# Performance work log

Measured on AMD Instinct MI355X. Metric: run time of the kernel, lower is better.

## Reference

```python
import jax, jax.numpy as jnp
import numpy as np

DIM = 1024
HEADS = 16
HEAD_DIM = DIM // HEADS
NEG = -1e30
EPS = 1e-5


def _linear(x, w, b):
    # torch nn.Linear: y = x @ W^T + b, W: [out, in]
    return jnp.einsum('bnd,od->bno', x, w) + b


def _mha(x, ctx, wq, bq, wk, bk, wv, bv, wo, bo, mask):
    B, N, D = x.shape
    M = ctx.shape[1]
    q = _linear(x, wq, bq).reshape(B, N, HEADS, HEAD_DIM).transpose(0, 2, 1, 3)
    k = _linear(ctx, wk, bk).reshape(B, M, HEADS, HEAD_DIM).transpose(0, 2, 1, 3)
    v = _linear(ctx, wv, bv).reshape(B, M, HEADS, HEAD_DIM).transpose(0, 2, 1, 3)
    scores = jnp.einsum('bhqd,bhkd->bhqk', q, k) / np.sqrt(HEAD_DIM).astype(np.float32)
    if mask is not None:
        scores = jnp.where(mask == 0, NEG, scores)
    attn = jax.nn.softmax(scores, axis=-1)  # dropout = identity (eval mode)
    out = jnp.einsum('bhqk,bhkd->bhqd', attn, v)
    out = out.transpose(0, 2, 1, 3).reshape(B, N, D)
    return _linear(out, wo, bo)


def _ln(x, g, b):
    mu = jnp.mean(x, axis=-1, keepdims=True)
    var = jnp.mean(jnp.square(x - mu), axis=-1, keepdims=True)
    return (x - mu) * jax.lax.rsqrt(var + EPS) * g + b


def setup_inputs() -> dict:
    key = jax.random.key(0)
    ks = jax.random.split(key, 24)
    B, N, M = 2, 2048, 1024
    s = 0.02
    d = {
        'x': jax.random.normal(ks[0], (B, N, DIM), jnp.float32),
        'memory': jax.random.normal(ks[1], (B, M, DIM), jnp.float32),
        'mask': jnp.tril(jnp.ones((N, N), jnp.int32))[None, None],
    }
    i = 2
    for p in ['sa', 'ca']:
        for nm in ['q', 'k', 'v', 'o']:
            d[f'{p}_w{nm}'] = jax.random.normal(ks[i], (DIM, DIM), jnp.float32) * s; i += 1
            d[f'{p}_b{nm}'] = jnp.zeros((DIM,), jnp.float32)
    d['ff_w1'] = jax.random.normal(ks[i], (4 * DIM, DIM), jnp.float32) * s; i += 1
    d['ff_b1'] = jnp.zeros((4 * DIM,), jnp.float32)
    d['ff_w2'] = jax.random.normal(ks[i], (DIM, 4 * DIM), jnp.float32) * s; i += 1
    d['ff_b2'] = jnp.zeros((DIM,), jnp.float32)
    for j in (1, 2, 3):
        d[f'ln{j}_g'] = jnp.ones((DIM,), jnp.float32)
        d[f'ln{j}_b'] = jnp.zeros((DIM,), jnp.float32)
    return d


def reference(x, memory, mask,
              sa_wq, sa_bq, sa_wk, sa_bk, sa_wv, sa_bv, sa_wo, sa_bo,
              ca_wq, ca_bq, ca_wk, ca_bk, ca_wv, ca_bv, ca_wo, ca_bo,
              ff_w1, ff_b1, ff_w2, ff_b2,
              ln1_g, ln1_b, ln2_g, ln2_b, ln3_g, ln3_b):
    x = _ln(x + _mha(x, x, sa_wq, sa_bq, sa_wk, sa_bk, sa_wv, sa_bv, sa_wo, sa_bo, mask), ln1_g, ln1_b)
    x = _ln(x + _mha(x, memory, ca_wq, ca_bq, ca_wk, ca_bk, ca_wv, ca_bv, ca_wo, ca_bo, None), ln2_g, ln2_b)
    h = jax.nn.relu(_linear(x, ff_w1, ff_b1))  # dropout = identity (eval)
    x = _ln(x + _linear(h, ff_w2, ff_b2), ln3_g, ln3_b)
    return x
```

## Files before the change

### kernel.cpp

```cpp
#include <hip/hip_runtime.h>


typedef __attribute__((ext_vector_type(8))) short bf16x8;
typedef __attribute__((ext_vector_type(4))) float f32x4;

__device__ __forceinline__ unsigned short f2bf(float f) {
    union { float f; unsigned int u; } v; v.f = f;
    unsigned int r = v.u + 0x7fffu + ((v.u >> 16) & 1u);
    return (unsigned short)(r >> 16);
}
__device__ __forceinline__ float bf2f(unsigned short u) {
    union { unsigned int u; float f; } v; v.u = (unsigned int)u << 16;
    return v.f;
}
__device__ __forceinline__ unsigned int bftrunc(float f) {
    union { float f; unsigned int u; } v; v.f = f;
    return v.u >> 16;
}

struct ConvArgs {
    const float* src[12];
    unsigned short* dst[12];
    int blk_ofs[13];
    int n4[12];
    const float* bq; const float* bk; const float* bv;
    const float* ck; const float* cv;
    float* bqkv; float* bkvc;
};
__global__ __launch_bounds__(256) void conv_multi(ConvArgs a)
{
    int bid = blockIdx.x;
    if (bid >= a.blk_ofs[12]) {
        int i = (bid - a.blk_ofs[12]) * 256 + threadIdx.x;
        if (i < 1024)       a.bqkv[i] = a.bq[i];
        else if (i < 2048)  a.bqkv[i] = a.bk[i - 1024];
        else if (i < 3072)  a.bqkv[i] = a.bv[i - 2048];
        else if (i < 4096)  a.bkvc[i - 3072] = a.ck[i - 3072];
        else if (i < 5120)  a.bkvc[i - 3072] = a.cv[i - 4096];
        return;
    }
    int s = 0;
#pragma unroll
    for (int t = 0; t < 12; ++t) if (bid >= a.blk_ofs[t + 1]) s = t + 1;
    int i = (bid - a.blk_ofs[s]) * 256 + threadIdx.x;
    if (i >= a.n4[s]) return;
    float4 v = ((const float4*)a.src[s])[i];
    ushort4 o;
    o.x = f2bf(v.x); o.y = f2bf(v.y); o.z = f2bf(v.z); o.w = f2bf(v.w);
    ((ushort4*)a.dst[s])[i] = o;
}

template<int TM, int TN, int EPI, int SK>
__device__ __forceinline__ void gemm_body(
    unsigned short (*As)[64], unsigned short (*Bs)[64],
    const unsigned short* __restrict__ A, const unsigned short* __restrict__ W,
    const float* __restrict__ bias, unsigned short* __restrict__ out,
    int K, int Ncols, long slice_stride, int bid, int gx, int zslice)
{
    constexpr int AI = TM / 32;
    constexpr int BJ = TN / 32;

    const int tid  = threadIdx.x;
    const int lane = tid & 63;
    const int wave = tid >> 6;
    const int qd   = lane >> 4;
    const int l15  = lane & 15;
    const int wm   = (wave >> 1) * (TM / 2);
    const int wn   = (wave & 1) * (TN / 2);

    const int gpg = 8 * gx;
    const long m0 = (long)((bid / gpg) * 8 + (bid & 7)) * TM;
    const long n0 = (long)((bid % gpg) >> 3) * TN;

    f32x4 acc[AI][BJ] = {};

    const int srow = lane >> 3;
    const int scol = (((lane & 7) ^ srow)) * 8;
    const unsigned short* Ag = A + (m0 + wave * (8 * AI) + srow) * (long)K + scol;
    const unsigned short* Wg = W + (n0 + wave * (8 * BJ) + srow) * (long)K + scol;

    const int ksl   = K / SK;
    const int kbase = (SK > 1) ? zslice * ksl : 0;

    for (int k0 = kbase; k0 < kbase + ksl; k0 += 64) {
#pragma unroll
        for (int c = 0; c < AI; ++c)
            __builtin_amdgcn_global_load_lds(
                (const __attribute__((address_space(1))) unsigned int*)(Ag + (long)c * 8 * K + k0),
                (__attribute__((address_space(3))) unsigned int*)((char*)&As[0][0] + (wave * AI + c) * 1024),
                16, 0, 0);
#pragma unroll
        for (int c = 0; c < BJ; ++c)
            __builtin_amdgcn_global_load_lds(
                (const __attribute__((address_space(1))) unsigned int*)(Wg + (long)c * 8 * K + k0),
                (__attribute__((address_space(3))) unsigned int*)((char*)&Bs[0][0] + (wave * BJ + c) * 1024),
                16, 0, 0);
        __syncthreads();
#pragma unroll
        for (int kk = 0; kk < 64; kk += 32) {
            const int pg = ((((kk >> 3) + qd)) ^ (l15 & 7)) * 8;
            bf16x8 af[AI], bw[BJ];
#pragma unroll
            for (int i = 0; i < AI; ++i)
                af[i] = *(const bf16x8*)&As[wm + i * 16 + l15][pg];
#pragma unroll
            for (int j = 0; j < BJ; ++j)
                bw[j] = *(const bf16x8*)&Bs[wn + j * 16 + l15][pg];
#pragma unroll
            for (int i = 0; i < AI; ++i)
#pragma unroll
                for (int j = 0; j < BJ; ++j)
                    acc[i][j] = __builtin_amdgcn_mfma_f32_16x16x32_bf16(
                        af[i], bw[j], acc[i][j], 0, 0, 0);
        }
        __syncthreads();
    }

    unsigned short* op = out + ((SK > 1) ? (long)zslice * slice_stride : 0);
#pragma unroll
    for (int j = 0; j < BJ; ++j) {
        long col = n0 + wn + j * 16 + l15;
        float bv = (SK == 1 || zslice == 0) ? bias[col] : 0.f;
#pragma unroll
        for (int i = 0; i < AI; ++i) {
#pragma unroll
            for (int r = 0; r < 4; ++r) {
                long row = m0 + wm + i * 16 + qd * 4 + r;
                float v = acc[i][j][r] + bv;
                if (EPI == 1) v = (v > 0.f) ? v : 0.f;
                op[row * Ncols + col] = f2bf(v);
            }
        }
    }
}

template<int TM, int TN, int EPI, int SK>
__global__ __launch_bounds__(256) void gemm_bt(
    const unsigned short* __restrict__ A, const unsigned short* __restrict__ W,
    const float* __restrict__ bias, unsigned short* __restrict__ out,
    int K, int Ncols, long slice_stride)
{
    __shared__ unsigned short As[TM][64];
    __shared__ unsigned short Bs[TN][64];
    const int bid = blockIdx.y * gridDim.x + blockIdx.x;
    gemm_body<TM, TN, EPI, SK>(As, Bs, A, W, bias, out, K, Ncols, slice_stride,
                               bid, gridDim.x, (int)blockIdx.z);
}

template<int EPI, int SK>
__device__ __forceinline__ void gemm8_body(
    unsigned short* Ab, unsigned short* Bb,
    const unsigned short* __restrict__ A, const unsigned short* __restrict__ W,
    const float* __restrict__ bias, unsigned short* __restrict__ out,
    int K, int Ncols, long slice_stride, int bid, int gx, int zslice)
{
    const int tid  = threadIdx.x;
    const int lane = tid & 63;
    const int wave = tid >> 6;
    const int qd   = lane >> 4;
    const int l15  = lane & 15;
    const int wm   = (wave >> 2) * 128;
    const int wn   = (wave & 3) * 64;

    const int gpg = 8 * gx;
    const long m0 = (long)((bid / gpg) * 8 + (bid & 7)) * 256;
    const long n0 = (long)((bid % gpg) >> 3) * 256;

    const int ksl   = K / SK;
    const int kbase = (SK > 1) ? zslice * ksl : 0;
    const int NG    = ksl / 64;

    f32x4 acc[8][4] = {};

    const int srow = tid >> 3;
    const int sgrp = ((tid & 7) ^ (srow & 7)) * 8;
    const unsigned short* Ag = A + (m0 + srow) * (long)K + kbase + sgrp;
    const unsigned short* Wg = W + (n0 + srow) * (long)K + kbase + sgrp;

    auto stA = [&](int db, int r0, int kt) {
        __builtin_amdgcn_global_load_lds(
            (const __attribute__((address_space(1))) unsigned int*)(Ag + (long)r0 * K + kt * 64),
            (__attribute__((address_space(3))) unsigned int*)(Ab + db * 16384 + r0 * 64 + wave * 512),
            16, 0, 0);
    };
    auto stB = [&](int db, int r0, int kt) {
        __builtin_amdgcn_global_load_lds(
            (const __attribute__((address_space(1))) unsigned int*)(Wg + (long)r0 * K + kt * 64),
            (__attribute__((address_space(3))) unsigned int*)(Bb + db * 16384 + r0 * 64 + wave * 512),
            16, 0, 0);
    };
    auto rdA = [&](int db, int row, int kk) -> bf16x8 {
        const int p = (((kk << 2) + qd) ^ (l15 & 7)) << 3;
        return *(const bf16x8*)(Ab + db * 16384 + row * 64 + p);
    };
    auto rdB = [&](int db, int row, int kk) -> bf16x8 {
        const int p = (((kk << 2) + qd) ^ (l15 & 7)) << 3;
        return *(const bf16x8*)(Bb + db * 16384 + row * 64 + p);
    };

#pragma unroll
    for (int h = 0; h < 4; ++h) stA(0, h * 64, 0);
#pragma unroll
    for (int h = 0; h < 4; ++h) stB(0, h * 64, 0);
    if (NG > 1) {
#pragma unroll
        for (int h = 0; h < 4; ++h) stA(1, h * 64, 1);
#pragma unroll
        for (int h = 0; h < 4; ++h) stB(1, h * 64, 1);
        asm volatile("s_waitcnt vmcnt(8)" ::: "memory");
    } else {
        asm volatile("s_waitcnt vmcnt(0)" ::: "memory");
    }
    __builtin_amdgcn_s_barrier();

    for (int g = 0; g < NG; ++g) {
        const int db = g & 1, nb = db ^ 1;
        const bool pf1 = (g >= 1) && (g + 1 < NG);
        const bool pf2 = (g + 2 < NG);
        bf16x8 af[4][2], bw[4][2];

#pragma unroll
        for (int i = 0; i < 4; ++i)
#pragma unroll
            for (int kk = 0; kk < 2; ++kk)
                af[i][kk] = rdA(db, wm + i * 16 + l15, kk);
#pragma unroll
        for (int j = 0; j < 2; ++j)
#pragma unroll
            for (int kk = 0; kk < 2; ++kk)
                bw[j][kk] = rdB(db, wn + j * 16 + l15, kk);
        if (pf1) { stA(nb, 64, g + 1); stA(nb, 192, g + 1); }
        __builtin_amdgcn_s_barrier();
        asm volatile("s_waitcnt lgkmcnt(0)" ::: "memory");
        __builtin_amdgcn_sched_barrier(0);
        __builtin_amdgcn_s_setprio(1);
#pragma unroll
        for (int i = 0; i < 4; ++i)
#pragma unroll
            for (int j = 0; j < 2; ++j) {
                acc[i][j] = __builtin_amdgcn_mfma_f32_16x16x32_bf16(af[i][0], bw[j][0], acc[i][j], 0, 0, 0);
                acc[i][j] = __builtin_amdgcn_mfma_f32_16x16x32_bf16(af[i][1], bw[j][1], acc[i][j], 0, 0, 0);
            }
        __builtin_amdgcn_s_setprio(0);
        __builtin_amdgcn_s_barrier();

#pragma unroll
        for (int j = 2; j < 4; ++j)
#pragma unroll
            for (int kk = 0; kk < 2; ++kk)
                bw[j][kk] = rdB(db, wn + j * 16 + l15, kk);
        if (pf1) { stB(nb, 0, g + 1); stB(nb, 64, g + 1); }
        __builtin_amdgcn_s_barrier();
        asm volatile("s_waitcnt lgkmcnt(0)" ::: "memory");
        __builtin_amdgcn_sched_barrier(0);
        __builtin_amdgcn_s_setprio(1);
#pragma unroll
        for (int i = 0; i < 4; ++i)
#pragma unroll
            for (int j = 2; j < 4; ++j) {
                acc[i][j] = __builtin_amdgcn_mfma_f32_16x16x32_bf16(af[i][0], bw[j][0], acc[i][j], 0, 0, 0);
                acc[i][j] = __builtin_amdgcn_mfma_f32_16x16x32_bf16(af[i][1], bw[j][1], acc[i][j], 0, 0, 0);
            }
        __builtin_amdgcn_s_setprio(0);
        __builtin_amdgcn_s_barrier();

#pragma unroll
        for (int i = 0; i < 4; ++i)
#pragma unroll
            for (int kk = 0; kk < 2; ++kk)
                af[i][kk] = rdA(db, wm + 64 + i * 16 + l15, kk);
        if (pf1) { stB(nb, 128, g + 1); stB(nb, 192, g + 1); }
        __builtin_amdgcn_s_barrier();
        asm volatile("s_waitcnt lgkmcnt(0)" ::: "memory");
        __builtin_amdgcn_sched_barrier(0);
        __builtin_amdgcn_s_setprio(1);
#pragma unroll
        for (int i = 0; i < 4; ++i)
#pragma unroll
            for (int j = 0; j < 2; ++j) {
                acc[4 + i][j] = __builtin_amdgcn_mfma_f32_16x16x32_bf16(af[i][0], bw[j][0], acc[4 + i][j], 0, 0, 0);
                acc[4 + i][j] = __builtin_amdgcn_mfma_f32_16x16x32_bf16(af[i][1], bw[j][1], acc[4 + i][j], 0, 0, 0);
            }
        __builtin_amdgcn_s_setprio(0);
        __builtin_amdgcn_s_barrier();

        if (pf2) { stA(db, 0, g + 2); stA(db, 128, g + 2); }
        __builtin_amdgcn_s_setprio(1);
#pragma unroll
        for (int i = 0; i < 4; ++i)
#pragma unroll
            for (int j = 2; j < 4; ++j) {
                acc[4 + i][j] = __builtin_amdgcn_mfma_f32_16x16x32_bf16(af[i][0], bw[j][0], acc[4 + i][j], 0, 0, 0);
                acc[4 + i][j] = __builtin_amdgcn_mfma_f32_16x16x32_bf16(af[i][1], bw[j][1], acc[4 + i][j], 0, 0, 0);
            }
        __builtin_amdgcn_s_setprio(0);
        if (pf2)             { asm volatile("s_waitcnt vmcnt(2)" ::: "memory"); }
        else if (g + 1 < NG) { asm volatile("s_waitcnt vmcnt(0)" ::: "memory"); }
        __builtin_amdgcn_s_barrier();
    }

    unsigned short* op = out + ((SK > 1) ? (long)zslice * slice_stride : 0);
#pragma unroll
    for (int j = 0; j < 4; ++j) {
        long col = n0 + wn + j * 16 + l15;
        float bv = (SK == 1 || zslice == 0) ? bias[col] : 0.f;
#pragma unroll
        for (int i = 0; i < 8; ++i) {
#pragma unroll
            for (int r = 0; r < 4; ++r) {
                long row = m0 + wm + (i >> 2) * 64 + (i & 3) * 16 + qd * 4 + r;
                float v = acc[i][j][r] + bv;
                if (EPI == 1) v = (v > 0.f) ? v : 0.f;
                op[row * Ncols + col] = f2bf(v);
            }
        }
    }
}

template<int EPI, int SK>
__global__ __launch_bounds__(512) void gemm8_bt(
    const unsigned short* __restrict__ A, const unsigned short* __restrict__ W,
    const float* __restrict__ bias, unsigned short* __restrict__ out,
    int K, int Ncols, long slice_stride)
{
    extern __shared__ unsigned short smem[];
    const int bid = blockIdx.y * gridDim.x + blockIdx.x;
    gemm8_body<EPI, SK>(smem, smem + 32768, A, W, bias, out, K, Ncols,
                        slice_stride, bid, gridDim.x, (int)blockIdx.z);
}

__global__ __launch_bounds__(512) void gemm8_dual(
    const unsigned short* A0, const unsigned short* W0, const float* b0,
    unsigned short* o0, int K0, int N0, int gx0, int nb0,
    const unsigned short* A1, const unsigned short* W1, const float* b1,
    unsigned short* o1, int K1, int N1, int gx1)
{
    extern __shared__ unsigned short smem[];
    const int bid = blockIdx.x;
    if (bid < nb0)
        gemm8_body<0, 1>(smem, smem + 32768, A0, W0, b0, o0, K0, N0, 0, bid, gx0, 0);
    else
        gemm8_body<0, 1>(smem, smem + 32768, A1, W1, b1, o1, K1, N1, 0, bid - nb0, gx1, 0);
}

__global__ __launch_bounds__(256) void attn_kernel(
    const unsigned short* __restrict__ Qb, int q_stride,
    const unsigned short* __restrict__ KVb, int kv_stride, int koff, int voff,
    unsigned short* __restrict__ O,
    int Nq, int Mk, int causal)
{
    __shared__ unsigned short Ks[64][72];
    __shared__ unsigned short Vs[64][72];
    __shared__ unsigned short Ps[4][16][72];

    const int tid  = threadIdx.x;
    const int lane = tid & 63;
    const int wave = tid >> 6;
    const int qd   = lane >> 4;
    const int l15  = lane & 15;
    const int h    = blockIdx.y;
    const int b    = blockIdx.z;
    int jq = blockIdx.x;
    if (causal && (b & 1)) jq = gridDim.x - 1 - jq;
    const int q0 = jq * 64;
    const int tb = q0 + wave * 16;

    bf16x8 aq0, aq1;
    {
        const unsigned short* qp =
            Qb + (long)(b * Nq + tb + l15) * q_stride + h * 64 + qd * 8;
        aq0 = *(const bf16x8*)qp;
        aq1 = *(const bf16x8*)(qp + 32);
    }

    float lpart[4] = {};
    f32x4 oacc[4] = {};

    const int krow = tid >> 3;
    const int kcol = (tid & 7) * 8;
    const int vj   = tid & 31;
    const int va_k = (vj & 15) + ((vj & 16) << 1);
    const int vfg  = (tid >> 5) * 8;
    const int vpc  = (va_k & 15) * 4 + (va_k >> 4);

    const unsigned short* Kg = KVb + (long)b * Mk * kv_stride + koff + h * 64;
    const unsigned short* Vg = KVb + (long)b * Mk * kv_stride + voff + h * 64;

    bf16x8 kr0, kr1, vra, vrb;
    auto prefetch = [&](int k0) {
        kr0 = *(const bf16x8*)(Kg + (long)(k0 + krow) * kv_stride + kcol);
        kr1 = *(const bf16x8*)(Kg + (long)(k0 + krow + 32) * kv_stride + kcol);
        const unsigned short* v0 = Vg + (long)(k0 + va_k) * kv_stride + vfg;
        vra = *(const bf16x8*)v0;
        vrb = *(const bf16x8*)(v0 + 16 * kv_stride);
    };

    const int nk = causal ? (q0 + 64) : Mk;
    prefetch(0);
    const float SCL = 0.125f * 1.44269504f;

    for (int k0 = 0; k0 < nk; k0 += 64) {
        __syncthreads();
        *(bf16x8*)&Ks[krow][kcol]      = kr0;
        *(bf16x8*)&Ks[krow + 32][kcol] = kr1;
#pragma unroll
        for (int jf = 0; jf < 8; ++jf) {
            unsigned int d = (unsigned short)vra[jf] |
                             ((unsigned int)(unsigned short)vrb[jf] << 16);
            *(unsigned int*)&Vs[vfg + jf][vpc] = d;
        }
        if (k0 + 64 < nk) prefetch(k0 + 64);
        __syncthreads();

        if (!causal || (k0 <= tb + 15)) {
            bf16x8 bk[4][2];
#pragma unroll
            for (int kt = 0; kt < 4; ++kt)
#pragma unroll
                for (int c = 0; c < 2; ++c)
                    bk[kt][c] = *(const bf16x8*)&Ks[kt * 16 + l15][c * 32 + qd * 8];
            f32x4 s[4];
#pragma unroll
            for (int kt = 0; kt < 4; ++kt) {
                f32x4 z = {};
                z = __builtin_amdgcn_mfma_f32_16x16x32_bf16(aq0, bk[kt][0], z, 0, 0, 0);
                z = __builtin_amdgcn_mfma_f32_16x16x32_bf16(aq1, bk[kt][1], z, 0, 0, 0);
                s[kt] = z;
            }
            const bool needmask = causal && (k0 + 63 > tb);
#pragma unroll
            for (int r = 0; r < 4; ++r) {
                const int qg = tb + qd * 4 + r;
                float e[4];
#pragma unroll
                for (int kt = 0; kt < 4; ++kt) {
                    float ev = __builtin_amdgcn_exp2f(s[kt][r] * SCL);
                    if (needmask && (k0 + kt * 16 + l15 > qg)) ev = 0.f;
                    e[kt] = ev;
                }
                lpart[r] += (e[0] + e[1]) + (e[2] + e[3]);
                unsigned int lo = bftrunc(e[0]) | (bftrunc(e[1]) << 16);
                unsigned int hi = bftrunc(e[2]) | (bftrunc(e[3]) << 16);
                uint2 pk; pk.x = lo; pk.y = hi;
                *(uint2*)&Ps[wave][qd * 4 + r][l15 * 4] = pk;
            }
            bf16x8 bv[4][2];
#pragma unroll
            for (int dt = 0; dt < 4; ++dt)
#pragma unroll
                for (int c = 0; c < 2; ++c)
                    bv[dt][c] = *(const bf16x8*)&Vs[dt * 16 + l15][c * 32 + qd * 8];
            bf16x8 ap0 = *(const bf16x8*)&Ps[wave][l15][qd * 8];
            bf16x8 ap1 = *(const bf16x8*)&Ps[wave][l15][32 + qd * 8];
#pragma unroll
            for (int dt = 0; dt < 4; ++dt) {
                oacc[dt] = __builtin_amdgcn_mfma_f32_16x16x32_bf16(
                    ap0, bv[dt][0], oacc[dt], 0, 0, 0);
                oacc[dt] = __builtin_amdgcn_mfma_f32_16x16x32_bf16(
                    ap1, bv[dt][1], oacc[dt], 0, 0, 0);
            }
        }
    }

#pragma unroll
    for (int r = 0; r < 4; ++r) {
        float l = lpart[r];
        l += __shfl_xor(l, 1);
        l += __shfl_xor(l, 2);
        l += __shfl_xor(l, 4);
        l += __shfl_xor(l, 8);
        float inv = 1.f / l;
        long row = (long)(b * Nq + tb + qd * 4 + r);
#pragma unroll
        for (int dt = 0; dt < 4; ++dt)
            O[row * 1024 + h * 64 + dt * 16 + l15] = f2bf(oacc[dt][r] * inv);
    }
}

template<int ND, int RESBF>
__global__ __launch_bounds__(256) void ln_res_kernel(
    const void* __restrict__ res, const unsigned short* __restrict__ delta,
    long dstride, const float* __restrict__ g, const float* __restrict__ beta,
    float* __restrict__ yout, unsigned short* __restrict__ ybf)
{
    __shared__ float red[8];
    const int row = blockIdx.x;
    const int tid = threadIdx.x;
    const long base = (long)row * 1024 + tid * 4;
    float v0, v1, v2, v3;
    if (RESBF) {
        ushort4 a = *(const ushort4*)((const unsigned short*)res + base);
        v0 = bf2f(a.x); v1 = bf2f(a.y); v2 = bf2f(a.z); v3 = bf2f(a.w);
    } else {
        float4 a = *(const float4*)((const float*)res + base);
        v0 = a.x; v1 = a.y; v2 = a.z; v3 = a.w;
    }
#pragma unroll
    for (int t = 0; t < ND; ++t) {
        ushort4 d = *(const ushort4*)(delta + t * dstride + base);
        v0 += bf2f(d.x); v1 += bf2f(d.y); v2 += bf2f(d.z); v3 += bf2f(d.w);
    }
    float s  = v0 + v1 + v2 + v3;
    float ss = v0 * v0 + v1 * v1 + v2 * v2 + v3 * v3;
#pragma unroll
    for (int off = 1; off < 64; off <<= 1) {
        s  += __shfl_xor(s, off);
        ss += __shfl_xor(ss, off);
    }
    const int wave = tid >> 6;
    if ((tid & 63) == 0) { red[wave] = s; red[4 + wave] = ss; }
    __syncthreads();
    float st  = red[0] + red[1] + red[2] + red[3];
    float sst = red[4] + red[5] + red[6] + red[7];
    float mean = st * (1.f / 1024.f);
    float var  = sst * (1.f / 1024.f) - mean * mean;
    float inv  = rsqrtf(var + 1e-5f);
    const int c = tid * 4;
    float y0 = (v0 - mean) * inv * g[c + 0] + beta[c + 0];
    float y1 = (v1 - mean) * inv * g[c + 1] + beta[c + 1];
    float y2 = (v2 - mean) * inv * g[c + 2] + beta[c + 2];
    float y3 = (v3 - mean) * inv * g[c + 3] + beta[c + 3];
    if (yout) *(float4*)(yout + base) = make_float4(y0, y1, y2, y3);
    if (ybf) {
        ushort4 o;
        o.x = f2bf(y0); o.y = f2bf(y1); o.z = f2bf(y2); o.w = f2bf(y3);
        *(ushort4*)(ybf + base) = o;
    }
}

extern "C" void kernel_launch(void* const* d_in, const int* in_sizes, int n_in,
                              void* d_out, int out_size, void* d_ws, size_t ws_size,
                              hipStream_t stream)
{
    const int B = 2, N = 2048, M = 1024, D = 1024, FF = 4096;
    const int TN = B * N;
    const int TM = B * M;
    const size_t MB = 1024 * 1024;

    const float* x     = (const float*)d_in[0];
    const float* mem   = (const float*)d_in[1];
    const float* sa_wq = (const float*)d_in[3];  const float* sa_bq = (const float*)d_in[4];
    const float* sa_wk = (const float*)d_in[5];  const float* sa_bk = (const float*)d_in[6];
    const float* sa_wv = (const float*)d_in[7];  const float* sa_bv = (const float*)d_in[8];
    const float* sa_wo = (const float*)d_in[9];  const float* sa_bo = (const float*)d_in[10];
    const float* ca_wq = (const float*)d_in[11]; const float* ca_bq = (const float*)d_in[12];
    const float* ca_wk = (const float*)d_in[13]; const float* ca_bk = (const float*)d_in[14];
    const float* ca_wv = (const float*)d_in[15]; const float* ca_bv = (const float*)d_in[16];
    const float* ca_wo = (const float*)d_in[17]; const float* ca_bo = (const float*)d_in[18];
    const float* ff_w1 = (const float*)d_in[19]; const float* ff_b1 = (const float*)d_in[20];
    const float* ff_w2 = (const float*)d_in[21]; const float* ff_b2 = (const float*)d_in[22];
    const float* ln1_g = (const float*)d_in[23]; const float* ln1_b = (const float*)d_in[24];
    const float* ln2_g = (const float*)d_in[25]; const float* ln2_b = (const float*)d_in[26];
    const float* ln3_g = (const float*)d_in[27]; const float* ln3_b = (const float*)d_in[28];

    char* w = (char*)d_ws;
    size_t off = 0;
    auto alloc = [&](size_t bytes) -> char* {
        char* p = w + off; off += (bytes + 255) & ~(size_t)255; return p;
    };

    unsigned short* xb   = (unsigned short*)alloc((size_t)TN * D * 2);
    unsigned short* memb = (unsigned short*)alloc((size_t)TM * D * 2);
    unsigned short* wqkv = (unsigned short*)alloc((size_t)3 * D * D * 2);
    unsigned short* wos  = (unsigned short*)alloc((size_t)D * D * 2);
    unsigned short* wqc  = (unsigned short*)alloc((size_t)D * D * 2);
    unsigned short* wkvc = (unsigned short*)alloc((size_t)2 * D * D * 2);
    unsigned short* woc  = (unsigned short*)alloc((size_t)D * D * 2);
    unsigned short* w1b  = (unsigned short*)alloc((size_t)FF * D * 2);
    unsigned short* w2b  = (unsigned short*)alloc((size_t)D * FF * 2);
    char* big = alloc((size_t)80 * MB);
    unsigned short* qkv   = (unsigned short*)big;
    unsigned short* ab    = (unsigned short*)(big + 24 * MB);
    unsigned short* kvb   = (unsigned short*)(big + 32 * MB);
    unsigned short* qb    = (unsigned short*)(big + 40 * MB);
    unsigned short* hb    = (unsigned short*)big;
    unsigned short* tmpbf = (unsigned short*)(big + 48 * MB);
    const long      TSL   = (long)TN * D;
    float* bqkv = (float*)alloc((size_t)3 * D * 4);
    float* bkvc = (float*)alloc((size_t)2 * D * 4);

    ConvArgs ca;
    const float* srcs[12] = {x, mem, sa_wq, sa_wk, sa_wv, sa_wo,
                             ca_wq, ca_wk, ca_wv, ca_wo, ff_w1, ff_w2};
    unsigned short* dsts[12] = {xb, memb, wqkv, wqkv + (size_t)D * D,
                                wqkv + (size_t)2 * D * D, wos, wqc, wkvc,
                                wkvc + (size_t)D * D, woc, w1b, w2b};
    long ns[12] = {(long)TN * D, (long)TM * D, (long)D * D, (long)D * D,
                   (long)D * D, (long)D * D, (long)D * D, (long)D * D,
                   (long)D * D, (long)D * D, (long)FF * D, (long)D * FF};
    int total_blk = 0;
    for (int i = 0; i < 12; ++i) {
        ca.src[i] = srcs[i]; ca.dst[i] = dsts[i];
        ca.n4[i] = (int)(ns[i] / 4);
        ca.blk_ofs[i] = total_blk;
        total_blk += (ca.n4[i] + 255) / 256;
    }
    ca.blk_ofs[12] = total_blk;
    ca.bq = sa_bq; ca.bk = sa_bk; ca.bv = sa_bv; ca.ck = ca_bk; ca.cv = ca_bv;
    ca.bqkv = bqkv; ca.bkvc = bkvc;
    conv_multi<<<dim3(total_blk + 20), dim3(256), 0, stream>>>(ca);

    dim3 blk(256);
    dim3 blk8(512);
    const unsigned int LDS8 = 131072;

    gemm8_dual<<<dim3(256), blk8, LDS8, stream>>>(
        xb,   wqkv, bqkv, qkv, D, 3 * D, 12, 192,
        memb, wkvc, bkvc, kvb, D, 2 * D, 8);

    attn_kernel<<<dim3(N / 64, 16, B), blk, 0, stream>>>(
        qkv, 3 * D, qkv, 3 * D, D, 2 * D, ab, N, N, 1);
    gemm_bt<128, 64, 0, 2><<<dim3(D / 64, TN / 128, 2), blk, 0, stream>>>(
        ab, wos, sa_bo, tmpbf, D, D, TSL);
    ln_res_kernel<2, 0><<<dim3(TN), blk, 0, stream>>>(
        x, tmpbf, TSL, ln1_g, ln1_b, nullptr, xb);

    gemm_bt<128, 64, 0, 1><<<dim3(D / 64, TN / 128), blk, 0, stream>>>(
        xb, wqc, ca_bq, qb, D, D, 0);
    attn_kernel<<<dim3(N / 64, 16, B), blk, 0, stream>>>(
        qb, D, kvb, 2 * D, 0, D, ab, N, M, 0);
    gemm_bt<128, 64, 0, 2><<<dim3(D / 64, TN / 128, 2), blk, 0, stream>>>(
        ab, woc, ca_bo, tmpbf, D, D, TSL);
    ln_res_kernel<2, 1><<<dim3(TN), blk, 0, stream>>>(
        xb, tmpbf, TSL, ln2_g, ln2_b, nullptr, xb);

    gemm8_bt<1, 1><<<dim3(FF / 256, TN / 256), blk8, LDS8, stream>>>(
        xb, w1b, ff_b1, hb, D, FF, 0);
    gemm8_bt<0, 4><<<dim3(D / 256, TN / 256, 4), blk8, LDS8, stream>>>(
        hb, w2b, ff_b2, tmpbf, FF, D, TSL);
    ln_res_kernel<4, 1><<<dim3(TN), blk, 0, stream>>>(
        xb, tmpbf, TSL, ln3_g, ln3_b, (float*)d_out, nullptr);
}
```

Measured before the change: 481.0 us.

## Remap GEMM block indices for XCD-aware L2 locality and swizzle attention LDS

The large GEMM kernels now derive tile coordinates from a flat block id, so that blocks landing on the same XCD (bid & 7) share M/N tile neighbourhoods. This is meant to improve L2 reuse across the chiplets. The attention kernel drops padded LDS rows (72 to 64 columns) in favour of XOR swizzling of K, V and P tiles, which cuts LDS footprint while avoiding bank conflicts. The hardcoded mappings assume the specific grid sizes (256 blocks, 16x16 or 12/8 tiles).

Result: faster. 461.2 us (-4.1%).

```diff
diff --git a/kernel.cpp b/kernel.cpp
--- a/kernel.cpp
+++ b/kernel.cpp
@@ -152,7 +152,7 @@
     unsigned short* Ab, unsigned short* Bb,
     const unsigned short* __restrict__ A, const unsigned short* __restrict__ W,
     const float* __restrict__ bias, unsigned short* __restrict__ out,
-    int K, int Ncols, long slice_stride, int bid, int gx, int zslice)
+    int K, int Ncols, long slice_stride, int mb, int nb, int zslice)
 {
     const int tid  = threadIdx.x;
     const int lane = tid & 63;
@@ -162,9 +162,8 @@
     const int wm   = (wave >> 2) * 128;
     const int wn   = (wave & 3) * 64;
 
-    const int gpg = 8 * gx;
-    const long m0 = (long)((bid / gpg) * 8 + (bid & 7)) * 256;
-    const long n0 = (long)((bid % gpg) >> 3) * 256;
+    const long m0 = (long)mb * 256;
+    const long n0 = (long)nb * 256;
 
     const int ksl   = K / SK;
     const int kbase = (SK > 1) ? zslice * ksl : 0;
@@ -214,7 +213,7 @@
     __builtin_amdgcn_s_barrier();
 
     for (int g = 0; g < NG; ++g) {
-        const int db = g & 1, nb = db ^ 1;
+        const int db = g & 1, nb2 = db ^ 1;
         const bool pf1 = (g >= 1) && (g + 1 < NG);
         const bool pf2 = (g + 2 < NG);
         bf16x8 af[4][2], bw[4][2];
@@ -229,7 +228,7 @@
 #pragma unroll
             for (int kk = 0; kk < 2; ++kk)
                 bw[j][kk] = rdB(db, wn + j * 16 + l15, kk);
-        if (pf1) { stA(nb, 64, g + 1); stA(nb, 192, g + 1); }
+        if (pf1) { stA(nb2, 64, g + 1); stA(nb2, 192, g + 1); }
         __builtin_amdgcn_s_barrier();
         asm volatile("s_waitcnt lgkmcnt(0)" ::: "memory");
         __builtin_amdgcn_sched_barrier(0);
@@ -249,7 +248,7 @@
 #pragma unroll
             for (int kk = 0; kk < 2; ++kk)
                 bw[j][kk] = rdB(db, wn + j * 16 + l15, kk);
-        if (pf1) { stB(nb, 0, g + 1); stB(nb, 64, g + 1); }
+        if (pf1) { stB(nb2, 0, g + 1); stB(nb2, 64, g + 1); }
         __builtin_amdgcn_s_barrier();
         asm volatile("s_waitcnt lgkmcnt(0)" ::: "memory");
         __builtin_amdgcn_sched_barrier(0);
@@ -269,7 +268,7 @@
 #pragma unroll
             for (int kk = 0; kk < 2; ++kk)
                 af[i][kk] = rdA(db, wm + 64 + i * 16 + l15, kk);
-        if (pf1) { stB(nb, 128, g + 1); stB(nb, 192, g + 1); }
+        if (pf1) { stB(nb2, 128, g + 1); stB(nb2, 192, g + 1); }
         __builtin_amdgcn_s_barrier();
         asm volatile("s_waitcnt lgkmcnt(0)" ::: "memory");
         __builtin_amdgcn_sched_barrier(0);
@@ -317,30 +316,49 @@
     }
 }
 
-template<int EPI, int SK>
+template<int EPI, int SK, int MODE>
 __global__ __launch_bounds__(512) void gemm8_bt(
     const unsigned short* __restrict__ A, const unsigned short* __restrict__ W,
     const float* __restrict__ bias, unsigned short* __restrict__ out,
     int K, int Ncols, long slice_stride)
 {
     extern __shared__ unsigned short smem[];
-    const int bid = blockIdx.y * gridDim.x + blockIdx.x;
+    const int bid = blockIdx.x;
+    const int x = bid & 7;
+    const int s = bid >> 3;
+    int mb, nb, z = 0;
+    if (MODE == 1) {
+        mb = (x >> 1) * 4 + (s & 3);
+        nb = (x & 1) * 8 + (s >> 2);
+    } else {
+        z  = x >> 1;
+        mb = (x & 1) * 8 + (s & 7);
+        nb = s >> 3;
+    }
     gemm8_body<EPI, SK>(smem, smem + 32768, A, W, bias, out, K, Ncols,
-                        slice_stride, bid, gridDim.x, (int)blockIdx.z);
+                        slice_stride, mb, nb, z);
 }
 
 __global__ __launch_bounds__(512) void gemm8_dual(
     const unsigned short* A0, const unsigned short* W0, const float* b0,
-    unsigned short* o0, int K0, int N0, int gx0, int nb0,
+    unsigned short* o0, int K0, int N0,
     const unsigned short* A1, const unsigned short* W1, const float* b1,
-    unsigned short* o1, int K1, int N1, int gx1)
+    unsigned short* o1, int K1, int N1)
 {
     extern __shared__ unsigned short smem[];
     const int bid = blockIdx.x;
-    if (bid < nb0)
-        gemm8_body<0, 1>(smem, smem + 32768, A0, W0, b0, o0, K0, N0, 0, bid, gx0, 0);
-    else
-        gemm8_body<0, 1>(smem, smem + 32768, A1, W1, b1, o1, K1, N1, 0, bid - nb0, gx1, 0);
+    const int x = bid & 7;
+    const int s = bid >> 3;
+    if (s < 24) {
+        const int mb = (x >> 1) * 4 + (s & 3);
+        const int nb = (x & 1) * 6 + (s >> 2);
+        gemm8_body<0, 1>(smem, smem + 32768, A0, W0, b0, o0, K0, N0, 0, mb, nb, 0);
+    } else {
+        const int t = s - 24;
+        const int mb = (x >> 1) * 2 + (t & 1);
+        const int nb = (x & 1) * 4 + (t >> 1);
+        gemm8_body<0, 1>(smem, smem + 32768, A1, W1, b1, o1, K1, N1, 0, mb, nb, 0);
+    }
 }
 
 __global__ __launch_bounds__(256) void attn_kernel(
@@ -349,15 +367,16 @@
     unsigned short* __restrict__ O,
     int Nq, int Mk, int causal)
 {
-    __shared__ unsigned short Ks[64][72];
-    __shared__ unsigned short Vs[64][72];
-    __shared__ unsigned short Ps[4][16][72];
+    __shared__ unsigned short Ks[64][64];
+    __shared__ unsigned short Vs[64][64];
+    __shared__ unsigned short Ps[4][16][64];
 
     const int tid  = threadIdx.x;
     const int lane = tid & 63;
     const int wave = tid >> 6;
     const int qd   = lane >> 4;
     const int l15  = lane & 15;
+    const int l7   = l15 & 7;
     const int h    = blockIdx.y;
     const int b    = blockIdx.z;
     int jq = blockIdx.x;
@@ -376,8 +395,9 @@
     float lpart[4] = {};
     f32x4 oacc[4] = {};
 
-    const int krow = tid >> 3;
-    const int kcol = (tid & 7) * 8;
+    const int krow  = tid >> 3;
+    const int kcol  = (tid & 7) * 8;
+    const int kcolS = (((tid & 7) ^ (krow & 7))) * 8;
     const int vj   = tid & 31;
     const int va_k = (vj & 15) + ((vj & 16) << 1);
     const int vfg  = (tid >> 5) * 8;
@@ -401,13 +421,14 @@
 
     for (int k0 = 0; k0 < nk; k0 += 64) {
         __syncthreads();
-        *(bf16x8*)&Ks[krow][kcol]      = kr0;
-        *(bf16x8*)&Ks[krow + 32][kcol] = kr1;
+        *(bf16x8*)&Ks[krow][kcolS]      = kr0;
+        *(bf16x8*)&Ks[krow + 32][kcolS] = kr1;
 #pragma unroll
         for (int jf = 0; jf < 8; ++jf) {
             unsigned int d = (unsigned short)vra[jf] |
                              ((unsigned int)(unsigned short)vrb[jf] << 16);
-            *(unsigned int*)&Vs[vfg + jf][vpc] = d;
+            const int row = vfg + jf;
+            *(unsigned int*)&Vs[row][vpc ^ ((row & 7) << 3)] = d;
         }
         if (k0 + 64 < nk) prefetch(k0 + 64);
         __syncthreads();
@@ -418,7 +439,7 @@
             for (int kt = 0; kt < 4; ++kt)
 #pragma unroll
                 for (int c = 0; c < 2; ++c)
-                    bk[kt][c] = *(const bf16x8*)&Ks[kt * 16 + l15][c * 32 + qd * 8];
+                    bk[kt][c] = *(const bf16x8*)&Ks[kt * 16 + l15][((c * 4 + qd) ^ l7) * 8];
             f32x4 s[4];
 #pragma unroll
             for (int kt = 0; kt < 4; ++kt) {
@@ -442,16 +463,17 @@
                 unsigned int lo = bftrunc(e[0]) | (bftrunc(e[1]) << 16);
                 unsigned int hi = bftrunc(e[2]) | (bftrunc(e[3]) << 16);
                 uint2 pk; pk.x = lo; pk.y = hi;
-                *(uint2*)&Ps[wave][qd * 4 + r][l15 * 4] = pk;
+                const int prow = qd * 4 + r;
+                *(uint2*)&Ps[wave][prow][(l15 * 4) ^ ((prow & 7) << 3)] = pk;
             }
             bf16x8 bv[4][2];
 #pragma unroll
             for (int dt = 0; dt < 4; ++dt)
 #pragma unroll
                 for (int c = 0; c < 2; ++c)
-                    bv[dt][c] = *(const bf16x8*)&Vs[dt * 16 + l15][c * 32 + qd * 8];
-            bf16x8 ap0 = *(const bf16x8*)&Ps[wave][l15][qd * 8];
-            bf16x8 ap1 = *(const bf16x8*)&Ps[wave][l15][32 + qd * 8];
+                    bv[dt][c] = *(const bf16x8*)&Vs[dt * 16 + l15][((c * 4 + qd) ^ l7) * 8];
+            bf16x8 ap0 = *(const bf16x8*)&Ps[wave][l15][(qd ^ l7) * 8];
+            bf16x8 ap1 = *(const bf16x8*)&Ps[wave][l15][((4 + qd) ^ l7) * 8];
 #pragma unroll
             for (int dt = 0; dt < 4; ++dt) {
                 oacc[dt] = __builtin_amdgcn_mfma_f32_16x16x32_bf16(
@@ -605,8 +627,8 @@
     const unsigned int LDS8 = 131072;
 
     gemm8_dual<<<dim3(256), blk8, LDS8, stream>>>(
-        xb,   wqkv, bqkv, qkv, D, 3 * D, 12, 192,
-        memb, wkvc, bkvc, kvb, D, 2 * D, 8);
+        xb,   wqkv, bqkv, qkv, D, 3 * D,
+        memb, wkvc, bkvc, kvb, D, 2 * D);
 
     attn_kernel<<<dim3(N / 64, 16, B), blk, 0, stream>>>(
         qkv, 3 * D, qkv, 3 * D, D, 2 * D, ab, N, N, 1);
@@ -624,9 +646,9 @@
     ln_res_kernel<2, 1><<<dim3(TN), blk, 0, stream>>>(
         xb, tmpbf, TSL, ln2_g, ln2_b, nullptr, xb);
 
-    gemm8_bt<1, 1><<<dim3(FF / 256, TN / 256), blk8, LDS8, stream>>>(
+    gemm8_bt<1, 1, 1><<<dim3(256), blk8, LDS8, stream>>>(
         xb, w1b, ff_b1, hb, D, FF, 0);
-    gemm8_bt<0, 4><<<dim3(D / 256, TN / 256, 4), blk8, LDS8, stream>>>(
+    gemm8_bt<0, 4, 2><<<dim3(256), blk8, LDS8, stream>>>(
         hb, w2b, ff_b2, tmpbf, FF, D, TSL);
     ln_res_kernel<4, 1><<<dim3(TN), blk, 0, stream>>>(
         xb, tmpbf, TSL, ln3_g, ln3_b, (float*)d_out, nullptr);
```
